# Kernel tuning notes

Measured on AMD Instinct MI355X. Metric: run time of the kernel, lower is better.

Reference implementation:

```python
import jax, jax.numpy as jnp
import numpy as np

B = 32; H = 56; W = 56; DIM = 384; HEADS = 12; WIN = 7; SHIFT = 3
HEAD_DIM = DIM // HEADS; SCALE = HEAD_DIM ** -0.5
N = WIN * WIN; NW = (H // WIN) * (W // WIN); L = H * W + 1; HID = 4 * DIM


def _rel_index():
    coords = np.stack(np.meshgrid(np.arange(WIN), np.arange(WIN), indexing='ij')).reshape(2, -1)
    rel = (coords[:, :, None] - coords[:, None, :]).transpose(1, 2, 0)
    rel[:, :, 0] += WIN - 1
    rel[:, :, 1] += WIN - 1
    rel[:, :, 0] *= 2 * WIN - 1
    return jnp.asarray(rel.sum(-1))  # (N, N) int


def _attn_mask():
    # standard Swin shift mask, padded with a zero column so the cls key is always visible
    img = np.zeros((H, W))
    sl = (slice(0, -WIN), slice(-WIN, -SHIFT), slice(-SHIFT, None))
    cnt = 0
    for hs in sl:
        for ws in sl:
            img[hs, ws] = cnt
            cnt += 1
    mw = img.reshape(H // WIN, WIN, W // WIN, WIN).transpose(0, 2, 1, 3).reshape(-1, N)
    m = mw[:, None, :] - mw[:, :, None]
    m = np.where(m != 0, -100.0, 0.0).astype(np.float32)
    m = np.pad(m, ((0, 0), (0, 0), (1, 0)))  # (nW, N, N+1)
    return jnp.asarray(m)


REL_INDEX = _rel_index()
ATTN_MASK = _attn_mask()


def _ln(x, g, b, eps=1e-5):
    m = x.mean(-1, keepdims=True)
    v = ((x - m) ** 2).mean(-1, keepdims=True)
    return (x - m) * jax.lax.rsqrt(v + eps) * g + b


def setup_inputs() -> dict:
    key = jax.random.key(0)
    ks = jax.random.split(key, 6)
    s = 0.02
    return dict(
        x=jax.random.normal(ks[0], (B, L, DIM), jnp.float32),
        norm1_g=jnp.ones((DIM,), jnp.float32), norm1_b=jnp.zeros((DIM,), jnp.float32),
        qkv_w=jax.random.normal(ks[1], (3 * DIM, DIM), jnp.float32) * s,
        qkv_b=jnp.zeros((3 * DIM,), jnp.float32),
        rel_bias_table=jax.random.normal(ks[2], ((2 * WIN - 1) ** 2, HEADS), jnp.float32) * s,
        proj_w=jax.random.normal(ks[3], (DIM, DIM), jnp.float32) * s,
        proj_b=jnp.zeros((DIM,), jnp.float32),
        norm2_g=jnp.ones((DIM,), jnp.float32), norm2_b=jnp.zeros((DIM,), jnp.float32),
        fc1_w=jax.random.normal(ks[4], (HID, DIM), jnp.float32) * s,
        fc1_b=jnp.zeros((HID,), jnp.float32),
        fc2_w=jax.random.normal(ks[5], (DIM, HID), jnp.float32) * s,
        fc2_b=jnp.zeros((DIM,), jnp.float32),
    )


def reference(x, norm1_g, norm1_b, qkv_w, qkv_b, rel_bias_table, proj_w, proj_b,
              norm2_g, norm2_b, fc1_w, fc1_b, fc2_w, fc2_b):
    Bx = x.shape[0]
    shortcut = x
    h = _ln(x, norm1_g, norm1_b)
    qkv = h @ qkv_w.T + qkv_b  # (B, L, 3C)

    # ---- global cls attention: token 0 attends to every token (ClsAttention) ----
    t = qkv.reshape(Bx, L, 3, HEADS, HEAD_DIM).transpose(2, 0, 3, 1, 4)  # (3, B, h, L, d)
    q0 = t[0, :, :, 0:1, :] * SCALE
    cls_attn = jax.nn.softmax(jnp.einsum('bhqd,bhkd->bhqk', q0, t[1]), axis=-1)
    cls_out = jnp.einsum('bhqk,bhkd->bhqd', cls_attn, t[2]).transpose(0, 2, 1, 3).reshape(Bx, 1, DIM)

    # ---- shifted-window attention for patch tokens, cls qkv prepended per window ----
    cls_qkv = qkv[:, :1]  # (B, 1, 3C)
    p = qkv[:, 1:].reshape(Bx, H, W, 3 * DIM)
    p = jnp.roll(p, (-SHIFT, -SHIFT), axis=(1, 2))
    pw = p.reshape(Bx, H // WIN, WIN, W // WIN, WIN, 3 * DIM).transpose(0, 1, 3, 2, 4, 5)
    pw = pw.reshape(Bx * NW, N, 3 * DIM)
    cls_rep = jnp.broadcast_to(cls_qkv[:, None], (Bx, NW, 1, 3 * DIM)).reshape(Bx * NW, 1, 3 * DIM)
    qkvw = jnp.concatenate([cls_rep, pw], axis=1)  # (B*nW, N+1, 3C)

    tw = qkvw.reshape(Bx * NW, N + 1, 3, HEADS, HEAD_DIM).transpose(2, 0, 3, 1, 4)
    q = tw[0, :, :, 1:, :] * SCALE  # patch queries (B*nW, h, N, d)
    attn = jnp.einsum('bhqd,bhkd->bhqk', q, tw[1])  # (B*nW, h, N, N+1)
    rel = rel_bias_table[REL_INDEX.reshape(-1)].reshape(N, N, HEADS).transpose(2, 0, 1)
    attn = jnp.concatenate([attn[..., :1], attn[..., 1:] + rel[None]], axis=-1)
    attn = attn.reshape(Bx, NW, HEADS, N, N + 1) + ATTN_MASK[None, :, None]
    attn = jax.nn.softmax(attn.reshape(Bx * NW, HEADS, N, N + 1), axis=-1)
    xw = jnp.einsum('bhqk,bhkd->bhqd', attn, tw[2]).transpose(0, 2, 1, 3).reshape(Bx * NW, N, DIM)

    # window reverse + reverse cyclic shift
    xp = xw.reshape(Bx, H // WIN, W // WIN, WIN, WIN, DIM).transpose(0, 1, 3, 2, 4, 5).reshape(Bx, H, W, DIM)
    xp = jnp.roll(xp, (SHIFT, SHIFT), axis=(1, 2)).reshape(Bx, H * W, DIM)

    a = jnp.concatenate([cls_out, xp], axis=1) @ proj_w.T + proj_b
    x1 = shortcut + a
    h2 = _ln(x1, norm2_g, norm2_b)
    h2 = jax.nn.gelu(h2 @ fc1_w.T + fc1_b, approximate=False)
    return x1 + (h2 @ fc2_w.T + fc2_b)
```

## Files before the change

kernel.cpp:

```cpp
#include <hip/hip_runtime.h>

#define DEVI __device__ __forceinline__

typedef __attribute__((ext_vector_type(8))) __bf16 bf16x8;
typedef __attribute__((ext_vector_type(4))) float f32x4;
typedef unsigned short u16;
typedef unsigned int u32;

static constexpr int kB = 32;
static constexpr int kL = 3137;
static constexpr int kM = kB * kL;
static constexpr int kHeads = 12;
static constexpr float kScale = 0.17677669529663687f;

DEVI u16 f2b(float f) {
  u32 u = __float_as_uint(f);
  u32 r = (u + 0x7fffu + ((u >> 16) & 1u)) >> 16;
  return (u16)r;
}
DEVI float blo(u32 u) { return __uint_as_float(u << 16); }
DEVI float bhi(u32 u) { return __uint_as_float(u & 0xffff0000u); }
DEVI float b2f(u16 h) { return __uint_as_float(((u32)h) << 16); }

DEVI void async16(const void* g, void* l) {
  __builtin_amdgcn_global_load_lds((const __attribute__((address_space(1))) u32*)g,
                                   (__attribute__((address_space(3))) u32*)l, 16, 0, 0);
}

DEVI float wred_max(float v) {
#pragma unroll
  for (int o = 32; o; o >>= 1) v = fmaxf(v, __shfl_xor(v, o));
  return v;
}
DEVI float wred_sum(float v) {
#pragma unroll
  for (int o = 32; o; o >>= 1) v += __shfl_xor(v, o);
  return v;
}

__global__ void cvt_all(const float* __restrict__ a, const float* __restrict__ b,
                        const float* __restrict__ c2, const float* __restrict__ d,
                        u16* __restrict__ oa, u16* __restrict__ ob,
                        u16* __restrict__ oc, u16* __restrict__ od) {
  int i = blockIdx.x * 256 + threadIdx.x;
  if (i < 442368) oa[i] = f2b(a[i]);
  else if (i < 589824) ob[i - 442368] = f2b(b[i - 442368]);
  else if (i < 1179648) oc[i - 589824] = f2b(c2[i - 589824]);
  else od[i - 1179648] = f2b(d[i - 1179648]);
}

__global__ __launch_bounds__(256)
void ln384(const float* __restrict__ x, const float* __restrict__ gam,
           const float* __restrict__ bet, u16* __restrict__ out, int rows) {
  int row = blockIdx.x * 4 + (threadIdx.x >> 6);
  if (row >= rows) return;
  int lane = threadIdx.x & 63;
  const float2* xr = (const float2*)(x + (size_t)row * 384);
  float2 v[3];
  float s = 0.f, s2 = 0.f;
#pragma unroll
  for (int i = 0; i < 3; i++) {
    v[i] = xr[lane + 64 * i];
    s += v[i].x + v[i].y;
    s2 += v[i].x * v[i].x + v[i].y * v[i].y;
  }
  s = wred_sum(s);
  s2 = wred_sum(s2);
  float mean = s * (1.f / 384.f);
  float var = s2 * (1.f / 384.f) - mean * mean;
  float rinv = rsqrtf(var + 1e-5f);
  const float2* gp = (const float2*)gam;
  const float2* bp = (const float2*)bet;
  u32* orow = (u32*)(out + (size_t)row * 384);
#pragma unroll
  for (int i = 0; i < 3; i++) {
    int idx = lane + 64 * i;
    float2 gg = gp[idx], bb = bp[idx];
    float lo = (v[i].x - mean) * rinv * gg.x + bb.x;
    float hi = (v[i].y - mean) * rinv * gg.y + bb.y;
    orow[idx] = (u32)f2b(lo) | ((u32)f2b(hi) << 16);
  }
}

__global__ __launch_bounds__(256)
void ln384b(const u16* __restrict__ x, const float* __restrict__ gam,
            const float* __restrict__ bet, u16* __restrict__ out, int rows) {
  int row = blockIdx.x * 4 + (threadIdx.x >> 6);
  if (row >= rows) return;
  int lane = threadIdx.x & 63;
  const u32* xr = (const u32*)(x + (size_t)row * 384);
  float vl[3], vh[3];
  float s = 0.f, s2 = 0.f;
#pragma unroll
  for (int i = 0; i < 3; i++) {
    u32 u = xr[lane + 64 * i];
    vl[i] = blo(u); vh[i] = bhi(u);
    s += vl[i] + vh[i];
    s2 += vl[i] * vl[i] + vh[i] * vh[i];
  }
  s = wred_sum(s);
  s2 = wred_sum(s2);
  float mean = s * (1.f / 384.f);
  float var = s2 * (1.f / 384.f) - mean * mean;
  float rinv = rsqrtf(var + 1e-5f);
  const float2* gp = (const float2*)gam;
  const float2* bp = (const float2*)bet;
  u32* orow = (u32*)(out + (size_t)row * 384);
#pragma unroll
  for (int i = 0; i < 3; i++) {
    int idx = lane + 64 * i;
    float2 gg = gp[idx], bb = bp[idx];
    float lo = (vl[i] - mean) * rinv * gg.x + bb.x;
    float hi = (vh[i] - mean) * rinv * gg.y + bb.y;
    orow[idx] = (u32)f2b(lo) | ((u32)f2b(hi) << 16);
  }
}

DEVI float gelu_exact(float v) { return 0.5f * v * (1.f + erff(v * 0.70710678118654752f)); }

template <int EPI>
__global__ __launch_bounds__(256)
void gemm_bt(const u16* __restrict__ A, const u16* __restrict__ W,
             const float* __restrict__ bias, const void* __restrict__ resv,
             void* __restrict__ outp, int M, int N, int K, int NX, int TMv) {
  const int nwg = gridDim.x;
  const int orig = blockIdx.x;
  const int xcd = orig & 7, rest = orig >> 3;
  const int q8 = nwg >> 3, r8 = nwg & 7;
  const int id = ((xcd < r8) ? xcd * (q8 + 1) : r8 * (q8 + 1) + (xcd - r8) * q8) + rest;
  const int col0 = (id % NX) * 128;
  const int rowG = (id / NX) * TMv * 128;

  const int tid = threadIdx.x, lane = tid & 63, wv = tid >> 6;
  __shared__ __align__(16) u16 As[3][128 * 32];
  __shared__ __align__(16) u16 Bs[3][128 * 32];
  const int wm = wv >> 1, wn = wv & 1;
  const int c = lane & 15, g = lane >> 4;
  const int NT = K >> 5;

  const int rr = lane >> 2;
  const int gnat = (lane & 3) ^ ((lane >> 3) & 3);

  auto stage = [&](int t2, int k2, int bfi) {
    int kk = k2 * 32 + gnat * 8;
    int rbase = rowG + t2 * 128;
#pragma unroll
    for (int s = 0; s < 2; s++) {
      int ch = wv * 2 + s;
      int r = ch * 16 + rr;
      async16(A + (size_t)min(rbase + r, M - 1) * K + kk, &As[bfi][ch * 512]);
      async16(W + (size_t)min(col0 + r, N - 1) * K + kk, &Bs[bfi][ch * 512]);
    }
  };

  int cc[4];
  float bv[4];
#pragma unroll
  for (int n = 0; n < 4; n++) {
    cc[n] = col0 + wn * 64 + n * 16 + c;
    bv[n] = bias[cc[n]];
  }

  stage(0, 0, 0);
  stage(0, 1, 1);
  int cur = 0;
  for (int t = 0; t < TMv; ++t) {
    f32x4 acc[4][4];
    f32x4 zero = {0.f, 0.f, 0.f, 0.f};
#pragma unroll
    for (int m = 0; m < 4; m++)
#pragma unroll
      for (int n = 0; n < 4; n++) acc[m][n] = zero;

    for (int kt = 0; kt < NT; ++kt) {
      if (t == TMv - 1 && kt == NT - 1) asm volatile("s_waitcnt vmcnt(0)" ::: "memory");
      else                              asm volatile("s_waitcnt vmcnt(4)" ::: "memory");
      __builtin_amdgcn_s_barrier();
      {
        int kt2 = kt + 2, t2 = t;
        if (kt2 >= NT) { kt2 -= NT; t2++; }
        if (t2 < TMv) {
          int nb = cur + 2; if (nb >= 3) nb -= 3;
          stage(t2, kt2, nb);
        }
      }
      bf16x8 af[4], bw[4];
#pragma unroll
      for (int m = 0; m < 4; m++) {
        int row = wm * 64 + m * 16 + c;
        af[m] = *(const bf16x8*)&As[cur][row * 32 + ((g ^ ((row >> 1) & 3)) << 3)];
      }
#pragma unroll
      for (int n = 0; n < 4; n++) {
        int row = wn * 64 + n * 16 + c;
        bw[n] = *(const bf16x8*)&Bs[cur][row * 32 + ((g ^ ((row >> 1) & 3)) << 3)];
      }
      __builtin_amdgcn_s_setprio(1);
#pragma unroll
      for (int m = 0; m < 4; m++)
#pragma unroll
        for (int n = 0; n < 4; n++)
          acc[m][n] = __builtin_amdgcn_mfma_f32_16x16x32_bf16(af[m], bw[n], acc[m][n], 0, 0, 0);
      __builtin_amdgcn_s_setprio(0);
      cur = cur + 1; if (cur >= 3) cur -= 3;
    }

    int rowT = rowG + t * 128;
#pragma unroll
    for (int m = 0; m < 4; m++) {
      int rb = rowT + wm * 64 + m * 16 + (g << 2);
#pragma unroll
      for (int j = 0; j < 4; j++) {
        int r = rb + j;
        if (r < M) {
#pragma unroll
          for (int n = 0; n < 4; n++) {
            float vv = acc[m][n][j] + bv[n];
            size_t off = (size_t)r * N + cc[n];
            if constexpr (EPI == 0) {
              ((u16*)outp)[off] = f2b(vv);
            } else if constexpr (EPI == 2) {
              ((u16*)outp)[off] = f2b(gelu_exact(vv));
            } else if constexpr (EPI == 3) {
              ((u16*)outp)[off] = f2b(vv + ((const float*)resv)[off]);
            } else {
              ((float*)outp)[off] = vv + b2f(((const u16*)resv)[off]);
            }
          }
        }
      }
    }
  }
}

__global__ __launch_bounds__(64)
void cls_reduce64(const float* __restrict__ parts, u16* __restrict__ aout) {
  int bh = blockIdx.x;
  int b = bh / kHeads, h = bh % kHeads;
  int lane = threadIdx.x;
  __shared__ float sm[64];
  const float* base = parts + (size_t)bh * 64 * 34;
  float m = base[lane * 34];
  float e = base[lane * 34 + 1];
  sm[lane] = m;
  float M = wred_max(m);
  float W = wred_sum(e * __expf(m - M));
  if (lane < 32) {
    float o = 0.f;
    for (int c2 = 0; c2 < 64; c2++)
      o += base[c2 * 34 + 2 + lane] * __expf(sm[c2] - M);
    aout[(size_t)b * kL * 384 + h * 32 + lane] = f2b(o / W);
  }
}

__global__ __launch_bounds__(256)
void bias_pre(const float* __restrict__ relb, float* __restrict__ bf) {
  int blk = blockIdx.x;
  int cls = blk / 12, h = blk % 12;
  int clsH = (cls >> 1) & 1, clsW = cls & 1;
  for (int idx = threadIdx.x; idx < 4096; idx += 256) {
    int k = idx >> 6, q = idx & 63;
    float v = 0.f;
    if (k >= 50) {
      v = -1e9f;
    } else if (k >= 1 && q < 49) {
      int kt = k - 1, ki = kt / 7, kj = kt % 7;
      int qi = q / 7, qj = q % 7;
      v = relb[((qi - ki + 6) * 13 + (qj - kj + 6)) * 12 + h];
      int rq = (clsH ? (qi < 4 ? 1 : 2) : 0) * 3 + (clsW ? (qj < 4 ? 1 : 2) : 0);
      int rk = (clsH ? (ki < 4 ? 1 : 2) : 0) * 3 + (clsW ? (kj < 4 ? 1 : 2) : 0);
      if (rq != rk) v -= 100.f;
    }
    bf[(size_t)blk * 4096 + idx] = v;
  }
}

__global__ __launch_bounds__(256)
void win_attn2(const u16* __restrict__ qkv, const float* __restrict__ biasf,
               u16* __restrict__ aout, float* __restrict__ parts) {
  const int tid = threadIdx.x, lane = tid & 63, wv = tid >> 6;
  const int gid = blockIdx.x * 4 + wv;
  const int h = gid % 12;
  const int wr = gid / 12;
  const int win = wr & 63, b = wr >> 6;
  const int wi = win >> 3, wj = win & 7;
  const int cls = ((wi == 7) ? 2 : 0) + ((wj == 7) ? 1 : 0);
  const int c = lane & 15, g = lane >> 4;

  __shared__ __align__(16) u16 KS[4][64 * 40];
  __shared__ __align__(16) u16 VT[4][32 * 72];
  __shared__ int RW[4][52];
  __shared__ float FP[4][52];
  u16* Ks = KS[wv];
  u16* Vt = VT[wv];
  int* Rows = RW[wv];
  float* Fp = FP[wv];

#pragma unroll
  for (int it = 0; it < 2; ++it) {
    int idx = it * 64 + lane;
    int tok = idx >> 1, half = idx & 1;
    if (tok < 50) {
      int row;
      if (tok == 0) {
        row = b * kL;
      } else {
        int n = tok - 1;
        int i = n / 7, j = n % 7;
        int r = wi * 7 + i, c2 = wj * 7 + j;
        int orr = r + 3; if (orr >= 56) orr -= 56;
        int occ = c2 + 3; if (occ >= 56) occ -= 56;
        row = b * kL + 1 + orr * 56 + occ;
      }
      if (half == 0) Rows[tok] = row;
      const u16* base = qkv + (size_t)row * 1152 + h * 32 + half * 16;
      uint4 k0 = *(const uint4*)(base + 384);
      uint4 k1 = *(const uint4*)(base + 384 + 8);
      *(uint4*)&Ks[tok * 40 + half * 16] = k0;
      *(uint4*)&Ks[tok * 40 + half * 16 + 8] = k1;
      uint4 v0 = *(const uint4*)(base + 768);
      uint4 v1 = *(const uint4*)(base + 768 + 8);
      u32 vw[8] = {v0.x, v0.y, v0.z, v0.w, v1.x, v1.y, v1.z, v1.w};
#pragma unroll
      for (int m = 0; m < 8; ++m) {
        Vt[(half * 16 + m * 2 + 0) * 72 + tok] = (u16)(vw[m] & 0xffffu);
        Vt[(half * 16 + m * 2 + 1) * 72 + tok] = (u16)(vw[m] >> 16);
      }
    } else {
      uint4 z = {0u, 0u, 0u, 0u};
      *(uint4*)&Ks[tok * 40 + half * 16] = z;
      *(uint4*)&Ks[tok * 40 + half * 16 + 8] = z;
#pragma unroll
      for (int m = 0; m < 16; ++m) Vt[(half * 16 + m) * 72 + tok] = 0;
    }
  }
  __syncthreads();

  {
    if (lane < 32)
      Fp[lane] = b2f(qkv[(size_t)(b * kL) * 1152 + h * 32 + lane]) * kScale;
    float sc = -1e30f;
    if (lane <= 49 && (lane >= 1 || win == 0)) {
      sc = 0.f;
      const u16* kr = &Ks[lane * 40];
#pragma unroll
      for (int d4 = 0; d4 < 4; d4++) {
        uint4 u = *(const uint4*)(kr + d4 * 8);
        sc += Fp[d4*8+0]*blo(u.x) + Fp[d4*8+1]*bhi(u.x)
            + Fp[d4*8+2]*blo(u.y) + Fp[d4*8+3]*bhi(u.y)
            + Fp[d4*8+4]*blo(u.z) + Fp[d4*8+5]*bhi(u.z)
            + Fp[d4*8+6]*blo(u.w) + Fp[d4*8+7]*bhi(u.w);
      }
    }
    float mloc = wred_max(sc);
    float pcls = (sc > -1e29f) ? __expf(sc - mloc) : 0.f;
    float esum = wred_sum(pcls);
    if (lane < 50) Fp[lane] = pcls;
    float* pp = parts + (size_t)((b * 12 + h) * 64 + win) * 34;
    if (lane == 0) { pp[0] = mloc; pp[1] = esum; }
    if (lane < 32) {
      float o = 0.f;
      for (int t = 0; t < 50; t++)
        o += Fp[t] * b2f(Vt[lane * 72 + t]);
      pp[2 + lane] = o;
    }
  }

  bf16x8 qf[4];
#pragma unroll
  for (int nt = 0; nt < 4; ++nt) {
    int q = nt * 16 + c;
    if (q > 48) q = 48;
    const u16* qp = qkv + (size_t)Rows[q + 1] * 1152 + h * 32 + g * 8;
    qf[nt] = *(const bf16x8*)qp;
  }

  f32x4 s[4][4];
  {
    f32x4 z = {0.f, 0.f, 0.f, 0.f};
    bf16x8 kf[4];
#pragma unroll
    for (int mt = 0; mt < 4; ++mt)
      kf[mt] = *(const bf16x8*)&Ks[(mt * 16 + c) * 40 + g * 8];
#pragma unroll
    for (int mt = 0; mt < 4; ++mt)
#pragma unroll
      for (int nt = 0; nt < 4; ++nt)
        s[mt][nt] = __builtin_amdgcn_mfma_f32_16x16x32_bf16(kf[mt], qf[nt], z, 0, 0, 0);
  }

  const float* bp = biasf + (size_t)(cls * 12 + h) * 4096;
  u32 wq[4][8];
#pragma unroll
  for (int nt = 0; nt < 4; ++nt) {
    float pv[16];
#pragma unroll
    for (int mt = 0; mt < 4; ++mt)
#pragma unroll
      for (int r = 0; r < 4; ++r)
        pv[mt * 4 + r] = s[mt][nt][r] * kScale + bp[(mt * 16 + g * 4 + r) * 64 + nt * 16 + c];
    float mx = pv[0];
#pragma unroll
    for (int i2 = 1; i2 < 16; ++i2) mx = fmaxf(mx, pv[i2]);
    mx = fmaxf(mx, __shfl_xor(mx, 16));
    mx = fmaxf(mx, __shfl_xor(mx, 32));
    float sum = 0.f;
#pragma unroll
    for (int i2 = 0; i2 < 16; ++i2) { pv[i2] = __expf(pv[i2] - mx); sum += pv[i2]; }
    sum += __shfl_xor(sum, 16);
    sum += __shfl_xor(sum, 32);
    float rs = 1.f / sum;
#pragma unroll
    for (int i2 = 0; i2 < 16; ++i2) pv[i2] *= rs;
#pragma unroll
    for (int mt = 0; mt < 4; ++mt) {
      u32 w0, w1;
      asm("v_cvt_pk_bf16_f32 %0, %1, %2" : "=v"(w0) : "v"(pv[mt * 4 + 0]), "v"(pv[mt * 4 + 1]));
      asm("v_cvt_pk_bf16_f32 %0, %1, %2" : "=v"(w1) : "v"(pv[mt * 4 + 2]), "v"(pv[mt * 4 + 3]));
      wq[nt][mt * 2 + 0] = w0;
      wq[nt][mt * 2 + 1] = w1;
    }
  }

  bf16x8 pa[4][2];
#pragma unroll
  for (int mt2 = 0; mt2 < 4; ++mt2)
#pragma unroll
    for (int ks = 0; ks < 2; ++ks) {
      union { u32 u[4]; bf16x8 v; } cvt;
#pragma unroll
      for (int wj2 = 0; wj2 < 4; ++wj2) {
        int srcLane = c + 16 * (((g & 1) << 1) + (wj2 >> 1));
        u32 a0 = (u32)__shfl((int)wq[mt2][(2 * ks + 0) * 2 + (wj2 & 1)], srcLane);
        u32 a1 = (u32)__shfl((int)wq[mt2][(2 * ks + 1) * 2 + (wj2 & 1)], srcLane);
        cvt.u[wj2] = (g < 2) ? a0 : a1;
      }
      pa[mt2][ks] = cvt.v;
    }

  f32x4 o[4][2];
  f32x4 z2 = {0.f, 0.f, 0.f, 0.f};
#pragma unroll
  for (int mt2 = 0; mt2 < 4; ++mt2)
#pragma unroll
    for (int ntd = 0; ntd < 2; ++ntd) o[mt2][ntd] = z2;
#pragma unroll
  for (int ks = 0; ks < 2; ++ks) {
    bf16x8 vf[2];
#pragma unroll
    for (int ntd = 0; ntd < 2; ++ntd)
      vf[ntd] = *(const bf16x8*)&Vt[(ntd * 16 + c) * 72 + ks * 32 + g * 8];
#pragma unroll
    for (int mt2 = 0; mt2 < 4; ++mt2)
#pragma unroll
      for (int ntd = 0; ntd < 2; ++ntd)
        o[mt2][ntd] = __builtin_amdgcn_mfma_f32_16x16x32_bf16(pa[mt2][ks], vf[ntd], o[mt2][ntd], 0, 0, 0);
  }

#pragma unroll
  for (int mt2 = 0; mt2 < 4; ++mt2)
#pragma unroll
    for (int r = 0; r < 4; ++r) {
      int q = mt2 * 16 + g * 4 + r;
      if (q < 49) {
        int row = Rows[q + 1];
        u16* op = aout + (size_t)row * 384 + h * 32 + c;
        op[0]  = f2b(o[mt2][0][r]);
        op[16] = f2b(o[mt2][1][r]);
      }
    }
}

extern "C" void kernel_launch(void* const* d_in, const int* in_sizes, int n_in,
                              void* d_out, int out_size, void* d_ws, size_t ws_size,
                              hipStream_t stream) {
  const float* x      = (const float*)d_in[0];
  const float* n1g    = (const float*)d_in[1];
  const float* n1b    = (const float*)d_in[2];
  const float* qkv_w  = (const float*)d_in[3];
  const float* qkv_b  = (const float*)d_in[4];
  const float* relb   = (const float*)d_in[5];
  const float* proj_w = (const float*)d_in[6];
  const float* proj_b = (const float*)d_in[7];
  const float* n2g    = (const float*)d_in[8];
  const float* n2b    = (const float*)d_in[9];
  const float* fc1_w  = (const float*)d_in[10];
  const float* fc1_b  = (const float*)d_in[11];
  const float* fc2_w  = (const float*)d_in[12];
  const float* fc2_b  = (const float*)d_in[13];
  float* out = (float*)d_out;
  char* ws = (char*)d_ws;

  u16* wqkv  = (u16*)(ws + 0);
  float* biasf = (float*)(ws + 0);
  u16* wproj = (u16*)(ws + 884736);
  u16* wfc1  = (u16*)(ws + 1179648);
  u16* wfc2  = (u16*)(ws + 2359296);
  u16* qkvb  = (u16*)(ws + 3538944);
  u16* x1b   = (u16*)(ws + 3538944);
  u16* h2b   = (u16*)(ws + 80633856);
  u16* gb    = (u16*)(ws + 119181312);
  u16* hbuf  = (u16*)(ws + 234823680);
  float* parts = (float*)d_out;

  cvt_all<<<6912, 256, 0, stream>>>(qkv_w, proj_w, fc1_w, fc2_w, wqkv, wproj, wfc1, wfc2);

  ln384<<<(kM + 3) / 4, 256, 0, stream>>>(x, n1g, n1b, hbuf, kM);
  gemm_bt<0><<<9 * 197, 256, 0, stream>>>(hbuf, wqkv, qkv_b, nullptr, qkvb, kM, 1152, 384, 9, 4);
  bias_pre<<<48, 256, 0, stream>>>(relb, biasf);
  win_attn2<<<kB * 64 * kHeads / 4, 256, 0, stream>>>(qkvb, biasf, hbuf, parts);
  cls_reduce64<<<kB * kHeads, 64, 0, stream>>>(parts, hbuf);
  gemm_bt<3><<<3 * 393, 256, 0, stream>>>(hbuf, wproj, proj_b, x, x1b, kM, 384, 384, 3, 2);

  for (int c = 0; c < 2; c++) {
    int r0 = c * 50192, nr = 50192;
    ln384b<<<(nr + 3) / 4, 256, 0, stream>>>(x1b + (size_t)r0 * 384, n2g, n2b, h2b, nr);
    gemm_bt<2><<<12 * 99, 256, 0, stream>>>(h2b, wfc1, fc1_b, nullptr, gb, nr, 1536, 384, 12, 4);
    gemm_bt<4><<<3 * 393, 256, 0, stream>>>(gb, wfc2, fc2_b, x1b + (size_t)r0 * 384,
                                            out + (size_t)r0 * 384, nr, 384, 1536, 3, 1);
  }
}
```

Baseline: 923.0 us.

## Drop multi-tile persistent GEMM loop and stage bf16 epilogue through LDS

Removes the per-block loop over several M tiles (TMv), so each workgroup computes one 128x128 tile and the grids grow to match. For bf16 outputs the epilogue now writes results into shared memory, then each lane stores 16-byte rows, and the fp32 residual is read as vectors. The aim is to replace scattered 2-byte global stores with coalesced wide ones. In exchange, prefetching no longer crosses tile boundaries, and the LDS round trip adds extra barriers.

```diff
diff --git a/kernel.cpp b/kernel.cpp
--- a/kernel.cpp
+++ b/kernel.cpp
@@ -122,14 +122,13 @@
 __global__ __launch_bounds__(256)
 void gemm_bt(const u16* __restrict__ A, const u16* __restrict__ W,
              const float* __restrict__ bias, const void* __restrict__ resv,
-             void* __restrict__ outp, int M, int N, int K, int NX, int TMv) {
+             void* __restrict__ outp, int M, int N, int K, int NX) {
   const int nwg = gridDim.x;
   const int orig = blockIdx.x;
   const int xcd = orig & 7, rest = orig >> 3;
   const int q8 = nwg >> 3, r8 = nwg & 7;
   const int id = ((xcd < r8) ? xcd * (q8 + 1) : r8 * (q8 + 1) + (xcd - r8) * q8) + rest;
-  const int col0 = (id % NX) * 128;
-  const int rowG = (id / NX) * TMv * 128;
+  const int col0 = (id % NX) * 128, row0 = (id / NX) * 128;
 
   const int tid = threadIdx.x, lane = tid & 63, wv = tid >> 6;
   __shared__ __align__(16) u16 As[3][128 * 32];
@@ -138,95 +137,122 @@
   const int c = lane & 15, g = lane >> 4;
   const int NT = K >> 5;
 
+  f32x4 acc[4][4];
+  f32x4 zero = {0.f, 0.f, 0.f, 0.f};
+#pragma unroll
+  for (int m = 0; m < 4; m++)
+#pragma unroll
+    for (int n = 0; n < 4; n++) acc[m][n] = zero;
+
   const int rr = lane >> 2;
   const int gnat = (lane & 3) ^ ((lane >> 3) & 3);
 
-  auto stage = [&](int t2, int k2, int bfi) {
-    int kk = k2 * 32 + gnat * 8;
-    int rbase = rowG + t2 * 128;
+  auto stage = [&](int kt, int bfi) {
+    int kk = kt * 32 + gnat * 8;
 #pragma unroll
     for (int s = 0; s < 2; s++) {
       int ch = wv * 2 + s;
       int r = ch * 16 + rr;
-      async16(A + (size_t)min(rbase + r, M - 1) * K + kk, &As[bfi][ch * 512]);
+      async16(A + (size_t)min(row0 + r, M - 1) * K + kk, &As[bfi][ch * 512]);
       async16(W + (size_t)min(col0 + r, N - 1) * K + kk, &Bs[bfi][ch * 512]);
     }
   };
 
-  int cc[4];
   float bv[4];
 #pragma unroll
-  for (int n = 0; n < 4; n++) {
-    cc[n] = col0 + wn * 64 + n * 16 + c;
-    bv[n] = bias[cc[n]];
-  }
-
-  stage(0, 0, 0);
-  stage(0, 1, 1);
+  for (int n = 0; n < 4; n++) bv[n] = bias[col0 + wn * 64 + n * 16 + c];
+
+  stage(0, 0);
+  stage(1, 1);
   int cur = 0;
-  for (int t = 0; t < TMv; ++t) {
-    f32x4 acc[4][4];
-    f32x4 zero = {0.f, 0.f, 0.f, 0.f};
+  for (int kt = 0; kt < NT; ++kt) {
+    if (kt + 1 < NT) asm volatile("s_waitcnt vmcnt(4)" ::: "memory");
+    else             asm volatile("s_waitcnt vmcnt(0)" ::: "memory");
+    __builtin_amdgcn_s_barrier();
+    if (kt + 2 < NT) {
+      int nb = cur + 2; if (nb >= 3) nb -= 3;
+      stage(kt + 2, nb);
+    }
+    bf16x8 af[4], bw[4];
+#pragma unroll
+    for (int m = 0; m < 4; m++) {
+      int row = wm * 64 + m * 16 + c;
+      af[m] = *(const bf16x8*)&As[cur][row * 32 + ((g ^ ((row >> 1) & 3)) << 3)];
+    }
+#pragma unroll
+    for (int n = 0; n < 4; n++) {
+      int row = wn * 64 + n * 16 + c;
+      bw[n] = *(const bf16x8*)&Bs[cur][row * 32 + ((g ^ ((row >> 1) & 3)) << 3)];
+    }
+    __builtin_amdgcn_s_setprio(1);
 #pragma unroll
     for (int m = 0; m < 4; m++)
 #pragma unroll
-      for (int n = 0; n < 4; n++) acc[m][n] = zero;
-
-    for (int kt = 0; kt < NT; ++kt) {
-      if (t == TMv - 1 && kt == NT - 1) asm volatile("s_waitcnt vmcnt(0)" ::: "memory");
-      else                              asm volatile("s_waitcnt vmcnt(4)" ::: "memory");
-      __builtin_amdgcn_s_barrier();
-      {
-        int kt2 = kt + 2, t2 = t;
-        if (kt2 >= NT) { kt2 -= NT; t2++; }
-        if (t2 < TMv) {
-          int nb = cur + 2; if (nb >= 3) nb -= 3;
-          stage(t2, kt2, nb);
-        }
-      }
-      bf16x8 af[4], bw[4];
-#pragma unroll
-      for (int m = 0; m < 4; m++) {
-        int row = wm * 64 + m * 16 + c;
-        af[m] = *(const bf16x8*)&As[cur][row * 32 + ((g ^ ((row >> 1) & 3)) << 3)];
-      }
-#pragma unroll
-      for (int n = 0; n < 4; n++) {
-        int row = wn * 64 + n * 16 + c;
-        bw[n] = *(const bf16x8*)&Bs[cur][row * 32 + ((g ^ ((row >> 1) & 3)) << 3)];
-      }
-      __builtin_amdgcn_s_setprio(1);
-#pragma unroll
-      for (int m = 0; m < 4; m++)
-#pragma unroll
-        for (int n = 0; n < 4; n++)
-          acc[m][n] = __builtin_amdgcn_mfma_f32_16x16x32_bf16(af[m], bw[n], acc[m][n], 0, 0, 0);
-      __builtin_amdgcn_s_setprio(0);
-      cur = cur + 1; if (cur >= 3) cur -= 3;
-    }
-
-    int rowT = rowG + t * 128;
+      for (int n = 0; n < 4; n++)
+        acc[m][n] = __builtin_amdgcn_mfma_f32_16x16x32_bf16(af[m], bw[n], acc[m][n], 0, 0, 0);
+    __builtin_amdgcn_s_setprio(0);
+    cur = cur + 1; if (cur >= 3) cur -= 3;
+  }
+
+  if constexpr (EPI == 4) {
 #pragma unroll
     for (int m = 0; m < 4; m++) {
-      int rb = rowT + wm * 64 + m * 16 + (g << 2);
+      int rb = row0 + wm * 64 + m * 16 + (g << 2);
 #pragma unroll
       for (int j = 0; j < 4; j++) {
         int r = rb + j;
         if (r < M) {
 #pragma unroll
           for (int n = 0; n < 4; n++) {
-            float vv = acc[m][n][j] + bv[n];
-            size_t off = (size_t)r * N + cc[n];
-            if constexpr (EPI == 0) {
-              ((u16*)outp)[off] = f2b(vv);
-            } else if constexpr (EPI == 2) {
-              ((u16*)outp)[off] = f2b(gelu_exact(vv));
-            } else if constexpr (EPI == 3) {
-              ((u16*)outp)[off] = f2b(vv + ((const float*)resv)[off]);
-            } else {
-              ((float*)outp)[off] = vv + b2f(((const u16*)resv)[off]);
-            }
+            size_t off = (size_t)r * N + col0 + wn * 64 + n * 16 + c;
+            ((float*)outp)[off] = acc[m][n][j] + bv[n] + b2f(((const u16*)resv)[off]);
           }
+        }
+      }
+    }
+  } else {
+    __syncthreads();
+    u16* T = (wv < 2) ? ((u16*)As + wv * 4608) : ((u16*)Bs + (wv - 2) * 4608);
+#pragma unroll
+    for (int m = 0; m < 4; m++)
+#pragma unroll
+      for (int j = 0; j < 4; j++) {
+        int rl = m * 16 + (g << 2) + j;
+#pragma unroll
+        for (int n = 0; n < 4; n++) {
+          float vv = acc[m][n][j] + bv[n];
+          u16 hv;
+          if constexpr (EPI == 2) hv = f2b(gelu_exact(vv));
+          else                    hv = f2b(vv);
+          T[rl * 72 + n * 16 + c] = hv;
+        }
+      }
+    __syncthreads();
+    const int l8 = lane & 7, rq8 = lane >> 3;
+    const int colB = col0 + wn * 64 + l8 * 8;
+#pragma unroll
+    for (int it = 0; it < 8; ++it) {
+      int rl = it * 8 + rq8;
+      int rg = row0 + wm * 64 + rl;
+      if (rg < M) {
+        uint4 q = *(const uint4*)&T[rl * 72 + l8 * 8];
+        size_t off = (size_t)rg * N + colB;
+        if constexpr (EPI == 3) {
+          const float* rp = (const float*)resv + off;
+          float4 ra = *(const float4*)rp;
+          float4 rb2 = *(const float4*)(rp + 4);
+          u32 w0 = (u32)f2b(b2f((u16)(q.x & 0xffff)) + ra.x) |
+                   ((u32)f2b(b2f((u16)(q.x >> 16)) + ra.y) << 16);
+          u32 w1 = (u32)f2b(b2f((u16)(q.y & 0xffff)) + ra.z) |
+                   ((u32)f2b(b2f((u16)(q.y >> 16)) + ra.w) << 16);
+          u32 w2 = (u32)f2b(b2f((u16)(q.z & 0xffff)) + rb2.x) |
+                   ((u32)f2b(b2f((u16)(q.z >> 16)) + rb2.y) << 16);
+          u32 w3 = (u32)f2b(b2f((u16)(q.w & 0xffff)) + rb2.z) |
+                   ((u32)f2b(b2f((u16)(q.w >> 16)) + rb2.w) << 16);
+          uint4 o4 = {w0, w1, w2, w3};
+          *(uint4*)((u16*)outp + off) = o4;
+        } else {
+          *(uint4*)((u16*)outp + off) = q;
         }
       }
     }
@@ -506,17 +532,17 @@
   cvt_all<<<6912, 256, 0, stream>>>(qkv_w, proj_w, fc1_w, fc2_w, wqkv, wproj, wfc1, wfc2);
 
   ln384<<<(kM + 3) / 4, 256, 0, stream>>>(x, n1g, n1b, hbuf, kM);
-  gemm_bt<0><<<9 * 197, 256, 0, stream>>>(hbuf, wqkv, qkv_b, nullptr, qkvb, kM, 1152, 384, 9, 4);
+  gemm_bt<0><<<9 * 785, 256, 0, stream>>>(hbuf, wqkv, qkv_b, nullptr, qkvb, kM, 1152, 384, 9);
   bias_pre<<<48, 256, 0, stream>>>(relb, biasf);
   win_attn2<<<kB * 64 * kHeads / 4, 256, 0, stream>>>(qkvb, biasf, hbuf, parts);
   cls_reduce64<<<kB * kHeads, 64, 0, stream>>>(parts, hbuf);
-  gemm_bt<3><<<3 * 393, 256, 0, stream>>>(hbuf, wproj, proj_b, x, x1b, kM, 384, 384, 3, 2);
+  gemm_bt<3><<<3 * 785, 256, 0, stream>>>(hbuf, wproj, proj_b, x, x1b, kM, 384, 384, 3);
 
   for (int c = 0; c < 2; c++) {
     int r0 = c * 50192, nr = 50192;
     ln384b<<<(nr + 3) / 4, 256, 0, stream>>>(x1b + (size_t)r0 * 384, n2g, n2b, h2b, nr);
-    gemm_bt<2><<<12 * 99, 256, 0, stream>>>(h2b, wfc1, fc1_b, nullptr, gb, nr, 1536, 384, 12, 4);
+    gemm_bt<2><<<12 * 393, 256, 0, stream>>>(h2b, wfc1, fc1_b, nullptr, gb, nr, 1536, 384, 12);
     gemm_bt<4><<<3 * 393, 256, 0, stream>>>(gb, wfc2, fc2_b, x1b + (size_t)r0 * 384,
-                                            out + (size_t)r0 * 384, nr, 384, 1536, 3, 1);
-  }
-}
+                                            out + (size_t)r0 * 384, nr, 384, 1536, 3);
+  }
+}
```

After: 889.3 us. -3.7%, faster.
